# Kernel tuning notes

Measured on AMD Instinct MI355X. Metric: run time of the kernel, lower is better.

The kernel has to match this reference:

```python
import jax, jax.numpy as jnp
import numpy as np

N, T, D_KQ, E_KQ, D_V, E_V, H = 2, 2048, 1024, 1024, 1024, 1024, 16


def setup_inputs() -> dict:
    key = jax.random.key(0)
    ks = jax.random.split(key, 12)
    def lin(k, fan_in, fan_out):
        return jax.random.normal(k, (fan_in, fan_out), jnp.float32) * (1.0 / np.sqrt(fan_in))
    return {
        "kq": jax.random.normal(ks[0], (N, T, D_KQ), jnp.float32),
        "v": jax.random.normal(ks[1], (N, T, D_V), jnp.float32),
        "Wk": lin(ks[2], D_KQ, E_KQ), "bk": jnp.zeros((E_KQ,), jnp.float32),
        "Wq": lin(ks[3], D_KQ, E_KQ), "bq": jnp.zeros((E_KQ,), jnp.float32),
        "Wv": lin(ks[4], D_V, E_V),   "bv": jnp.zeros((E_V,), jnp.float32),
        "W1": lin(ks[5], E_V, 4 * E_V), "b1": jnp.zeros((4 * E_V,), jnp.float32),
        "W2": lin(ks[6], 4 * E_V, E_V), "b2": jnp.zeros((E_V,), jnp.float32),
    }


def _shifted_causal_mask(T):
    # triu(-inf, diagonal=0): block j >= i (strictly-past attention), except [0,0] unmasked
    row = jnp.arange(T)[:, None]
    col = jnp.arange(T)[None, :]
    mask = jnp.where(col < row, 0.0, -jnp.inf).astype(jnp.float32)
    return mask.at[0, 0].set(0.0)


def reference(kq, v, Wk, bk, Wq, bq, Wv, bv, W1, b1, W2, b2):
    n, T, _ = kq.shape
    hd_kq = E_KQ // H
    hd_v = E_V // H
    # projections -> [n, H, T, hd]
    k = (kq @ Wk + bk).reshape(n, T, H, hd_kq).transpose(0, 2, 1, 3)
    q = (kq @ Wq + bq).reshape(n, T, H, hd_kq).transpose(0, 2, 1, 3)
    vv = (v @ Wv + bv).reshape(n, T, H, hd_v).transpose(0, 2, 1, 3)
    # NOTE: no 1/sqrt(d) scaling, faithful to source
    scores = jnp.einsum("bhqd,bhkd->bhqk", q, k) + _shifted_causal_mask(T)
    attn = jax.nn.softmax(scores, axis=-1)
    out = jnp.einsum("bhqk,bhkd->bhqd", attn, vv)
    out = out.transpose(0, 2, 1, 3).reshape(n, T, E_V)
    # GELU FFN (torch nn.GELU default = exact erf form)
    h = jax.nn.gelu(out @ W1 + b1, approximate=False)
    return h @ W2 + b2
```

## Files before the change

kernel.cpp:

```cpp
#include <hip/hip_runtime.h>

typedef short bf16x8 __attribute__((ext_vector_type(8)));
typedef unsigned short u16x8 __attribute__((ext_vector_type(8)));
typedef float f32x4 __attribute__((ext_vector_type(4)));
typedef unsigned short u16;

#define MFMA16(a, b, c) __builtin_amdgcn_mfma_f32_16x16x32_bf16((a), (b), (c), 0, 0, 0)
#define VMCNT0() asm volatile("s_waitcnt vmcnt(0)" ::: "memory")

__device__ __forceinline__ u16 bf16_rtn(float f) {
  unsigned u = __float_as_uint(f);
  u += 0x7fffu + ((u >> 16) & 1u);
  return (u16)(u >> 16);
}
__device__ __forceinline__ float bf16_to_f(u16 h) {
  return __uint_as_float(((unsigned)h) << 16);
}
__device__ __forceinline__ void splitf(float f, u16& hi, u16& lo) {
  hi = bf16_rtn(f);
  lo = bf16_rtn(f - bf16_to_f(hi));
}
__device__ __forceinline__ void gload16(const void* g, void* l) {
  __builtin_amdgcn_global_load_lds(
      (const __attribute__((address_space(1))) unsigned int*)g,
      (__attribute__((address_space(3))) unsigned int*)l, 16, 0, 0);
}
__device__ __forceinline__ float exp2_hw(float x) {
  float r;
  asm("v_exp_f32 %0, %1" : "=v"(r) : "v"(x));
  return r;
}
__device__ __forceinline__ void swz_bid(int& bx, int& by) {
  int gx = gridDim.x;
  int lin = (int)blockIdx.y * gx + (int)blockIdx.x;
  int cpx = (gx * (int)gridDim.y) >> 3;
  int nl = (lin & 7) * cpx + (lin >> 3);
  bx = nl % gx;
  by = nl / gx;
}

__global__ void k_cvt(const float* __restrict__ a, const float* __restrict__ b,
                      u16* __restrict__ hi, u16* __restrict__ lo,
                      u16* __restrict__ vb) {
  int i = blockIdx.x * blockDim.x + threadIdx.x;
  const int N4 = 1 << 20;
  if (i < N4) {
    float4 v4 = ((const float4*)a)[i];
    ushort4 h, l;
    splitf(v4.x, h.x, l.x);
    splitf(v4.y, h.y, l.y);
    splitf(v4.z, h.z, l.z);
    splitf(v4.w, h.w, l.w);
    ((ushort4*)hi)[i] = h;
    ((ushort4*)lo)[i] = l;
  } else {
    int j = i - N4;
    float4 v4 = ((const float4*)b)[j];
    ushort4 h;
    h.x = bf16_rtn(v4.x);
    h.y = bf16_rtn(v4.y);
    h.z = bf16_rtn(v4.z);
    h.w = bf16_rtn(v4.w);
    ((ushort4*)vb)[j] = h;
  }
}

template <int SPLIT>
__global__ void k_tconv(const float* __restrict__ in, u16* __restrict__ hi,
                        u16* __restrict__ lo, int R, int C) {
  __shared__ float tile[32][33];
  int c0 = blockIdx.x * 32, r0 = blockIdx.y * 32;
  int tx = threadIdx.x & 31, ty = threadIdx.x >> 5;
#pragma unroll
  for (int i = 0; i < 4; ++i)
    tile[ty + i * 8][tx] = in[(size_t)(r0 + ty + i * 8) * C + c0 + tx];
  __syncthreads();
#pragma unroll
  for (int i = 0; i < 4; ++i) {
    float v = tile[tx][ty + i * 8];
    size_t o = (size_t)(c0 + ty + i * 8) * R + r0 + tx;
    if (SPLIT) {
      u16 h, l;
      splitf(v, h, l);
      hi[o] = h;
      lo[o] = l;
    } else {
      hi[o] = bf16_rtn(v);
    }
  }
}

template <int GELU, int OUT, int BN>
__global__ __launch_bounds__(256) void k_gemm(
    const u16* __restrict__ A, const u16* __restrict__ B,
    const float* __restrict__ bias, void* __restrict__ C0,
    int M, int Nc, int K) {
  extern __shared__ u16 sm[];
  const int NB = BN / 32;
  const int BUFE = 8192 + BN * 64;

  int bx, by;
  swz_bid(bx, by);
  int m0 = by * 128, n0 = bx * BN;
  int t = threadIdx.x, lane = t & 63, w = t >> 6;
  int wr = (w >> 1) * 64, wc = (w & 1) * (BN / 2);
  int li = lane & 15, g = lane >> 4;
  int lrow = lane >> 3, lcg = lane & 7;

  f32x4 acc[4][4] = {};
  const int nk = K >> 6;

  auto stage = [&](int kb, int buf) {
    int k0 = kb * 64;
    u16* base = sm + buf * BUFE;
#pragma unroll
    for (int j = 0; j < 4; ++j) {
      int jj = w * 4 + j;
      int row = jj * 8 + lrow;
      int cg = lcg ^ (row & 7);
      gload16(A + (size_t)(m0 + row) * K + k0 + cg * 8, base + jj * 512);
    }
#pragma unroll
    for (int j = 0; j < NB; ++j) {
      int jj = w * NB + j;
      int row = jj * 8 + lrow;
      int cg = lcg ^ (row & 7);
      gload16(B + (size_t)(n0 + row) * K + k0 + cg * 8, base + 8192 + jj * 512);
    }
  };

  stage(0, 0);
  VMCNT0();
  __syncthreads();

  int cur = 0;
  for (int kb = 0; kb < nk; ++kb) {
    if (kb + 1 < nk) stage(kb + 1, cur ^ 1);
    const u16* bs = sm + cur * BUFE;
#pragma unroll
    for (int kk = 0; kk < 2; ++kk) {
      bf16x8 af[4], bf[4];
#pragma unroll
      for (int i = 0; i < 4; ++i) {
        int row = wr + i * 16 + li;
        af[i] = *(const bf16x8*)&bs[row * 64 + (((kk * 4 + g) ^ (li & 7)) << 3)];
      }
#pragma unroll
      for (int b = 0; b < NB; ++b) {
        int row = wc + b * 16 + li;
        bf[b] = *(const bf16x8*)&bs[8192 + row * 64 + (((kk * 4 + g) ^ (li & 7)) << 3)];
      }
#pragma unroll
      for (int a = 0; a < 4; ++a)
#pragma unroll
        for (int b = 0; b < NB; ++b) acc[a][b] = MFMA16(af[a], bf[b], acc[a][b]);
    }
    VMCNT0();
    __syncthreads();
    cur ^= 1;
  }

#pragma unroll
  for (int a = 0; a < 4; ++a)
#pragma unroll
    for (int b = 0; b < NB; ++b)
#pragma unroll
      for (int r = 0; r < 4; ++r) {
        int row = m0 + wr + a * 16 + g * 4 + r;
        int col = n0 + wc + b * 16 + li;
        float v = acc[a][b][r] + bias[col];
        if (GELU) v = 0.5f * v * (1.0f + erff(v * 0.70710678118654752f));
        if (OUT == 0) {
          ((float*)C0)[(size_t)row * Nc + col] = v;
        } else if (OUT == 1) {
          ((u16*)C0)[(size_t)row * Nc + col] = bf16_rtn(v);
        } else if (OUT == 5) {
          int nn = row >> 11, tt = row & 2047, kbb = tt >> 6, tr = tt & 63;
          int hq = col >> 6, d = col & 63;
          size_t base = (((size_t)nn * 16 + hq) * 32 + kbb) * 8192 + 4096;
          size_t ov = base + d * 64 + (tr & 7) + (((tr >> 3) ^ (d & 7)) << 3);
          ((u16*)C0)[ov] = bf16_rtn(v);
        }
      }
}

__global__ __launch_bounds__(256) void k_gemm_s(
    const u16* __restrict__ Ahi, const u16* __restrict__ Alo,
    const u16* __restrict__ Bhi, const u16* __restrict__ Blo,
    const float* __restrict__ bias, const float* __restrict__ bias2,
    void* __restrict__ C0, void* __restrict__ C1, void* __restrict__ C2,
    int M, int Nc, int K) {
  extern __shared__ u16 sm[];
  const int BUFE = 16384;

  int bx, by;
  swz_bid(bx, by);
  int m0 = by * 128, n0 = bx * 128;
  int t = threadIdx.x, lane = t & 63, w = t >> 6;
  int wr = (w >> 1) * 64, wc = (w & 1) * 64;
  int li = lane & 15, g = lane >> 4;
  int srow = lane >> 2, scol = (lane & 3) * 8;

  f32x4 acc[4][4] = {};
  const int nk = K >> 5;

  auto stage = [&](int kb, int buf) {
    int k0 = kb * 32;
    int bo = buf * BUFE;
#pragma unroll
    for (int c = 0; c < 2; ++c) {
      int row = w * 32 + c * 16 + srow;
      int ldso = bo + w * 1024 + c * 512;
      gload16(Ahi + (size_t)(m0 + row) * K + k0 + scol, sm + ldso);
      gload16(Bhi + (size_t)(n0 + row) * K + k0 + scol, sm + 4096 + ldso);
      gload16(Alo + (size_t)(m0 + row) * K + k0 + scol, sm + 8192 + ldso);
      gload16(Blo + (size_t)(n0 + row) * K + k0 + scol, sm + 12288 + ldso);
    }
  };

  stage(0, 0);
  VMCNT0();
  __syncthreads();

  int cur = 0;
  for (int kb = 0; kb < nk; ++kb) {
    if (kb + 1 < nk) stage(kb + 1, cur ^ 1);
    const u16* lA = sm + cur * BUFE;
    bf16x8 af[4], bfr[4], afl[4], bfl[4];
#pragma unroll
    for (int i = 0; i < 4; ++i) {
      af[i] = *(const bf16x8*)&lA[(wr + i * 16 + li) * 32 + g * 8];
      bfr[i] = *(const bf16x8*)&lA[4096 + (wc + i * 16 + li) * 32 + g * 8];
      afl[i] = *(const bf16x8*)&lA[8192 + (wr + i * 16 + li) * 32 + g * 8];
      bfl[i] = *(const bf16x8*)&lA[12288 + (wc + i * 16 + li) * 32 + g * 8];
    }
#pragma unroll
    for (int a = 0; a < 4; ++a)
#pragma unroll
      for (int b = 0; b < 4; ++b) {
        acc[a][b] = MFMA16(af[a], bfr[b], acc[a][b]);
        acc[a][b] = MFMA16(af[a], bfl[b], acc[a][b]);
        acc[a][b] = MFMA16(afl[a], bfr[b], acc[a][b]);
      }
    VMCNT0();
    __syncthreads();
    cur ^= 1;
  }

#pragma unroll
  for (int a = 0; a < 4; ++a)
#pragma unroll
    for (int b = 0; b < 4; ++b)
#pragma unroll
      for (int r = 0; r < 4; ++r) {
        int row = m0 + wr + a * 16 + g * 4 + r;
        int col = n0 + wc + b * 16 + li;
        float bb = col < 1024 ? bias[col] : bias2[col - 1024];
        float v = acc[a][b][r] + bb;
        if (col < 1024) {
          int nn = row >> 11, tt = row & 2047, kbb = tt >> 6, tr = tt & 63;
          int hq = col >> 6, d = col & 63, ks = d >> 5, dc = d & 31;
          size_t base = (((size_t)nn * 16 + hq) * 32 + kbb) * 8192;
          size_t oh = base + ks * 2048 + tr * 32 + (dc & 7) +
                      (((dc >> 3) ^ ((tr >> 1) & 3)) << 3);
          ((u16*)C0)[oh] = bf16_rtn(v);
        } else {
          int cq = col - 1024;
          float vq = v * 1.4426950408889634f;
          u16 hh, ll;
          splitf(vq, hh, ll);
          size_t off = (((size_t)(row >> 11) * 16 + (cq >> 6)) * 2048 + (row & 2047)) * 64 + (cq & 63);
          ((u16*)C1)[off] = hh;
          ((u16*)C2)[off] = ll;
        }
      }
}

__global__ __launch_bounds__(512) void k_attn(
    const u16* __restrict__ Qh, const u16* __restrict__ Ql,
    const u16* __restrict__ KV, u16* __restrict__ out) {
  const int T = 2048, HD = 64, H = 16, E = 1024;
  int hc = blockIdx.x;
  int h = hc & 15, n = hc >> 4;
  int qq = 15 - (int)blockIdx.y;
  __shared__ u16 KB[2][8192];
  __shared__ u16 P[2][128][36];
  int t = threadIdx.x, lane = t & 63, w = t >> 6;
  int li = lane & 15, g = lane >> 4;

  const size_t nh = (size_t)n * H + h;
  const u16* qhb = Qh + (nh * 2048 + (size_t)qq * 128) * 64;
  const u16* qlb = Ql + (nh * 2048 + (size_t)qq * 128) * 64;
  const u16* kvb = KV + nh * 32 * 8192;

  bf16x8 qh[2], ql[2];
#pragma unroll
  for (int ks = 0; ks < 2; ++ks) {
    qh[ks] = *(const bf16x8*)&qhb[(w * 16 + li) * 64 + ks * 32 + g * 8];
    ql[ks] = *(const bf16x8*)&qlb[(w * 16 + li) * 64 + ks * 32 + g * 8];
  }

#pragma unroll
  for (int j = 0; j < 2; ++j)
    gload16(kvb + (w * 2 + j) * 512 + lane * 8, &KB[0][(w * 2 + j) * 512]);
  VMCNT0();
  __syncthreads();

  float lr[4] = {0.f, 0.f, 0.f, 0.f};
  f32x4 O[4] = {};
  int cur = 0;
  const int nkb = 2 * qq + 2;

  for (int kb = 0; kb < nkb; ++kb) {
    if (kb + 1 < nkb) {
      const u16* src = kvb + (size_t)(kb + 1) * 8192 + (w * 2) * 512 + lane * 8;
#pragma unroll
      for (int j = 0; j < 2; ++j)
        gload16(src + j * 512, &KB[cur ^ 1][(w * 2 + j) * 512]);
    }

    f32x4 s[4] = {};
#pragma unroll
    for (int ks = 0; ks < 2; ++ks)
#pragma unroll
      for (int c = 0; c < 4; ++c) {
        int jr = c * 16 + li;
        int sw = (jr >> 1) & 3;
        bf16x8 kh = *(const bf16x8*)&KB[cur][ks * 2048 + jr * 32 + ((g ^ sw) << 3)];
        s[c] = MFMA16(qh[ks], kh, s[c]);
        s[c] = MFMA16(ql[ks], kh, s[c]);
      }

    if (kb >= 2 * qq) {
#pragma unroll
      for (int c = 0; c < 4; ++c)
#pragma unroll
        for (int r = 0; r < 4; ++r) {
          int i = qq * 128 + w * 16 + g * 4 + r;
          int j = kb * 64 + c * 16 + li;
          if (!(j < i || (i == 0 && j == 0))) s[c][r] = -INFINITY;
        }
    }

#pragma unroll
    for (int c = 0; c < 4; ++c)
#pragma unroll
      for (int r = 0; r < 4; ++r) {
        float p = exp2_hw(s[c][r]);
        s[c][r] = p;
        lr[r] += p;
      }

#pragma unroll
    for (int c = 0; c < 4; ++c)
#pragma unroll
      for (int r = 0; r < 4; ++r)
        P[c >> 1][w * 16 + g * 4 + r][(c & 1) * 16 + li] = bf16_rtn(s[c][r]);

#pragma unroll
    for (int ks = 0; ks < 2; ++ks) {
      bf16x8 pa = *(const bf16x8*)&P[ks][w * 16 + li][g * 8];
#pragma unroll
      for (int c = 0; c < 4; ++c) {
        int d = c * 16 + li;
        int tc = ks * 4 + g;
        bf16x8 vb = *(const bf16x8*)&KB[cur][4096 + d * 64 + ((tc ^ (d & 7)) << 3)];
        O[c] = MFMA16(pa, vb, O[c]);
      }
    }
    VMCNT0();
    __syncthreads();
    cur ^= 1;
  }

#pragma unroll
  for (int off = 1; off < 16; off <<= 1)
#pragma unroll
    for (int r = 0; r < 4; ++r) lr[r] += __shfl_xor(lr[r], off, 16);

#pragma unroll
  for (int c = 0; c < 4; ++c)
#pragma unroll
    for (int r = 0; r < 4; ++r) {
      float v = O[c][r] / lr[r];
      size_t row = (size_t)n * T + qq * 128 + w * 16 + g * 4 + r;
      out[row * E + h * HD + c * 16 + li] = bf16_rtn(v);
    }
}

extern "C" void kernel_launch(void* const* d_in, const int* in_sizes, int n_in,
                              void* d_out, int out_size, void* d_ws, size_t ws_size,
                              hipStream_t stream) {
  const float* kq = (const float*)d_in[0];
  const float* v = (const float*)d_in[1];
  const float* Wk = (const float*)d_in[2];
  const float* bk = (const float*)d_in[3];
  const float* Wq = (const float*)d_in[4];
  const float* bq = (const float*)d_in[5];
  const float* Wv = (const float*)d_in[6];
  const float* bv = (const float*)d_in[7];
  const float* W1 = (const float*)d_in[8];
  const float* b1 = (const float*)d_in[9];
  const float* W2 = (const float*)d_in[10];
  const float* b2 = (const float*)d_in[11];
  float* outp = (float*)d_out;

  char* ws = (char*)d_ws;
  u16* kq_hi = (u16*)(ws + 0);
  u16* kq_lo = (u16*)(ws + 8388608);
  u16* v_bf = (u16*)(ws + 16777216);
  u16* hbuf = (u16*)(ws + 0);
  u16* WkqT_hi = (u16*)(ws + 33554432);
  u16* WkqT_lo = (u16*)(ws + 37748736);
  u16* WvT = (u16*)(ws + 41943040);
  u16* W1T = (u16*)(ws + 44040192);
  u16* W2T = (u16*)(ws + 52428800);
  u16* Qh = (u16*)(ws + 60817408);
  u16* Ql = (u16*)(ws + 69206016);
  u16* KV = (u16*)(ws + 77594624);
  u16* attn_o = (u16*)(ws + 102760448);

  k_cvt<<<8192, 256, 0, stream>>>(kq, v, kq_hi, kq_lo, v_bf);
  k_tconv<1><<<dim3(32, 32), 256, 0, stream>>>(Wk, WkqT_hi, WkqT_lo, 1024, 1024);
  k_tconv<1><<<dim3(32, 32), 256, 0, stream>>>(Wq, WkqT_hi + (1 << 20), WkqT_lo + (1 << 20), 1024, 1024);
  k_tconv<0><<<dim3(32, 32), 256, 0, stream>>>(Wv, WvT, nullptr, 1024, 1024);
  k_tconv<0><<<dim3(128, 32), 256, 0, stream>>>(W1, W1T, nullptr, 1024, 4096);
  k_tconv<0><<<dim3(32, 128), 256, 0, stream>>>(W2, W2T, nullptr, 4096, 1024);

  k_gemm_s<<<dim3(16, 32), 256, 65536, stream>>>(
      kq_hi, kq_lo, WkqT_hi, WkqT_lo, bk, bq, KV, Qh, Ql, 4096, 2048, 1024);
  k_gemm<0, 5, 64><<<dim3(16, 32), 256, 49152, stream>>>(
      v_bf, WvT, bv, KV, 4096, 1024, 1024);

  k_attn<<<dim3(32, 16), 512, 0, stream>>>(Qh, Ql, KV, attn_o);

  k_gemm<1, 1, 128><<<dim3(32, 32), 256, 65536, stream>>>(
      attn_o, W1T, b1, hbuf, 4096, 4096, 1024);
  k_gemm<0, 0, 64><<<dim3(16, 32), 256, 49152, stream>>>(
      hbuf, W2T, b2, outp, 4096, 1024, 4096);
}
```

Measured before the change: 250.5 us.

## Triple-buffer GEMM and attention loads, drop activation lo-split, fuse weight transposes

Moves the GEMMs and the attention kernel from double to triple buffering in LDS, with a partial vmcnt wait so two stages are in flight at once. The K/Q projection no longer splits the kq activation into hi/lo, which removes one MFMA per tile and a quarter of the staged loads but lowers input precision. The Wk/Wq/Wv transposes merge into one launch, the k_gemm_s LDS layout gains an XOR swizzle, and the FFN1 GEMM tile width drops from 128 to 64. Static shared arrays replace dynamic LDS, and the larger footprint may reduce occupancy.

```diff
diff --git a/kernel.cpp b/kernel.cpp
--- a/kernel.cpp
+++ b/kernel.cpp
@@ -7,6 +7,7 @@
 
 #define MFMA16(a, b, c) __builtin_amdgcn_mfma_f32_16x16x32_bf16((a), (b), (c), 0, 0, 0)
 #define VMCNT0() asm volatile("s_waitcnt vmcnt(0)" ::: "memory")
+#define VMCNTN(n) asm volatile("s_waitcnt vmcnt(" #n ")" ::: "memory")
 
 __device__ __forceinline__ u16 bf16_rtn(float f) {
   unsigned u = __float_as_uint(f);
@@ -40,54 +41,60 @@
 }
 
 __global__ void k_cvt(const float* __restrict__ a, const float* __restrict__ b,
-                      u16* __restrict__ hi, u16* __restrict__ lo,
-                      u16* __restrict__ vb) {
+                      u16* __restrict__ ah, u16* __restrict__ vb) {
   int i = blockIdx.x * blockDim.x + threadIdx.x;
   const int N4 = 1 << 20;
-  if (i < N4) {
-    float4 v4 = ((const float4*)a)[i];
-    ushort4 h, l;
-    splitf(v4.x, h.x, l.x);
-    splitf(v4.y, h.y, l.y);
-    splitf(v4.z, h.z, l.z);
-    splitf(v4.w, h.w, l.w);
-    ((ushort4*)hi)[i] = h;
-    ((ushort4*)lo)[i] = l;
-  } else {
-    int j = i - N4;
-    float4 v4 = ((const float4*)b)[j];
-    ushort4 h;
-    h.x = bf16_rtn(v4.x);
-    h.y = bf16_rtn(v4.y);
-    h.z = bf16_rtn(v4.z);
-    h.w = bf16_rtn(v4.w);
-    ((ushort4*)vb)[j] = h;
-  }
-}
-
-template <int SPLIT>
-__global__ void k_tconv(const float* __restrict__ in, u16* __restrict__ hi,
-                        u16* __restrict__ lo, int R, int C) {
+  const float4 v4 = (i < N4) ? ((const float4*)a)[i] : ((const float4*)b)[i - N4];
+  ushort4 h;
+  h.x = bf16_rtn(v4.x);
+  h.y = bf16_rtn(v4.y);
+  h.z = bf16_rtn(v4.z);
+  h.w = bf16_rtn(v4.w);
+  if (i < N4)
+    ((ushort4*)ah)[i] = h;
+  else
+    ((ushort4*)vb)[i - N4] = h;
+}
+
+__global__ void k_tconvW(const float* __restrict__ Wk, const float* __restrict__ Wq,
+                         const float* __restrict__ Wv, u16* __restrict__ hi,
+                         u16* __restrict__ lo, u16* __restrict__ wvt) {
+  int z = blockIdx.z;
+  const float* in = (z == 0) ? Wk : (z == 1) ? Wq : Wv;
   __shared__ float tile[32][33];
   int c0 = blockIdx.x * 32, r0 = blockIdx.y * 32;
   int tx = threadIdx.x & 31, ty = threadIdx.x >> 5;
 #pragma unroll
   for (int i = 0; i < 4; ++i)
+    tile[ty + i * 8][tx] = in[(size_t)(r0 + ty + i * 8) * 1024 + c0 + tx];
+  __syncthreads();
+#pragma unroll
+  for (int i = 0; i < 4; ++i) {
+    float v = tile[tx][ty + i * 8];
+    size_t o = (size_t)(c0 + ty + i * 8) * 1024 + r0 + tx;
+    if (z < 2) {
+      u16 h, l;
+      splitf(v, h, l);
+      hi[(size_t)z * 1048576 + o] = h;
+      lo[(size_t)z * 1048576 + o] = l;
+    } else {
+      wvt[o] = bf16_rtn(v);
+    }
+  }
+}
+
+__global__ void k_tconv(const float* __restrict__ in, u16* __restrict__ hi,
+                        int R, int C) {
+  __shared__ float tile[32][33];
+  int c0 = blockIdx.x * 32, r0 = blockIdx.y * 32;
+  int tx = threadIdx.x & 31, ty = threadIdx.x >> 5;
+#pragma unroll
+  for (int i = 0; i < 4; ++i)
     tile[ty + i * 8][tx] = in[(size_t)(r0 + ty + i * 8) * C + c0 + tx];
   __syncthreads();
 #pragma unroll
-  for (int i = 0; i < 4; ++i) {
-    float v = tile[tx][ty + i * 8];
-    size_t o = (size_t)(c0 + ty + i * 8) * R + r0 + tx;
-    if (SPLIT) {
-      u16 h, l;
-      splitf(v, h, l);
-      hi[o] = h;
-      lo[o] = l;
-    } else {
-      hi[o] = bf16_rtn(v);
-    }
-  }
+  for (int i = 0; i < 4; ++i)
+    hi[(size_t)(c0 + ty + i * 8) * R + r0 + tx] = bf16_rtn(tile[tx][ty + i * 8]);
 }
 
 template <int GELU, int OUT, int BN>
@@ -95,9 +102,9 @@
     const u16* __restrict__ A, const u16* __restrict__ B,
     const float* __restrict__ bias, void* __restrict__ C0,
     int M, int Nc, int K) {
-  extern __shared__ u16 sm[];
   const int NB = BN / 32;
   const int BUFE = 8192 + BN * 64;
+  __shared__ u16 sm[3 * BUFE];
 
   int bx, by;
   swz_bid(bx, by);
@@ -107,7 +114,7 @@
   int li = lane & 15, g = lane >> 4;
   int lrow = lane >> 3, lcg = lane & 7;
 
-  f32x4 acc[4][4] = {};
+  f32x4 acc[4][NB] = {};
   const int nk = K >> 6;
 
   auto stage = [&](int kb, int buf) {
@@ -130,16 +137,20 @@
   };
 
   stage(0, 0);
-  VMCNT0();
+  stage(1, 1);
+  VMCNTN(6);
   __syncthreads();
 
   int cur = 0;
   for (int kb = 0; kb < nk; ++kb) {
-    if (kb + 1 < nk) stage(kb + 1, cur ^ 1);
+    int stb = cur + 2;
+    if (stb >= 3) stb -= 3;
+    if (kb + 2 < nk) stage(kb + 2, stb);
+
     const u16* bs = sm + cur * BUFE;
 #pragma unroll
     for (int kk = 0; kk < 2; ++kk) {
-      bf16x8 af[4], bf[4];
+      bf16x8 af[4], bf[NB];
 #pragma unroll
       for (int i = 0; i < 4; ++i) {
         int row = wr + i * 16 + li;
@@ -155,9 +166,13 @@
 #pragma unroll
         for (int b = 0; b < NB; ++b) acc[a][b] = MFMA16(af[a], bf[b], acc[a][b]);
     }
-    VMCNT0();
+    if (kb + 2 < nk) {
+      VMCNTN(6);
+    } else {
+      VMCNT0();
+    }
     __syncthreads();
-    cur ^= 1;
+    cur = (cur == 2) ? 0 : cur + 1;
   }
 
 #pragma unroll
@@ -185,13 +200,12 @@
 }
 
 __global__ __launch_bounds__(256) void k_gemm_s(
-    const u16* __restrict__ Ahi, const u16* __restrict__ Alo,
-    const u16* __restrict__ Bhi, const u16* __restrict__ Blo,
-    const float* __restrict__ bias, const float* __restrict__ bias2,
-    void* __restrict__ C0, void* __restrict__ C1, void* __restrict__ C2,
-    int M, int Nc, int K) {
-  extern __shared__ u16 sm[];
-  const int BUFE = 16384;
+    const u16* __restrict__ Ahi, const u16* __restrict__ Bhi,
+    const u16* __restrict__ Blo, const float* __restrict__ bias,
+    const float* __restrict__ bias2, void* __restrict__ C0,
+    void* __restrict__ C1, void* __restrict__ C2, int M, int Nc, int K) {
+  const int BUFE = 12288;
+  __shared__ u16 sm[3 * BUFE];
 
   int bx, by;
   swz_bid(bx, by);
@@ -199,40 +213,44 @@
   int t = threadIdx.x, lane = t & 63, w = t >> 6;
   int wr = (w >> 1) * 64, wc = (w & 1) * 64;
   int li = lane & 15, g = lane >> 4;
-  int srow = lane >> 2, scol = (lane & 3) * 8;
+  int srow = lane >> 2;
+  int sc = ((lane & 3) ^ ((srow >> 1) & 3)) * 8;
 
   f32x4 acc[4][4] = {};
   const int nk = K >> 5;
 
   auto stage = [&](int kb, int buf) {
     int k0 = kb * 32;
-    int bo = buf * BUFE;
+    u16* base = sm + buf * BUFE;
 #pragma unroll
     for (int c = 0; c < 2; ++c) {
       int row = w * 32 + c * 16 + srow;
-      int ldso = bo + w * 1024 + c * 512;
-      gload16(Ahi + (size_t)(m0 + row) * K + k0 + scol, sm + ldso);
-      gload16(Bhi + (size_t)(n0 + row) * K + k0 + scol, sm + 4096 + ldso);
-      gload16(Alo + (size_t)(m0 + row) * K + k0 + scol, sm + 8192 + ldso);
-      gload16(Blo + (size_t)(n0 + row) * K + k0 + scol, sm + 12288 + ldso);
+      int ldso = w * 1024 + c * 512;
+      gload16(Ahi + (size_t)(m0 + row) * K + k0 + sc, base + ldso);
+      gload16(Bhi + (size_t)(n0 + row) * K + k0 + sc, base + 4096 + ldso);
+      gload16(Blo + (size_t)(n0 + row) * K + k0 + sc, base + 8192 + ldso);
     }
   };
 
   stage(0, 0);
-  VMCNT0();
+  stage(1, 1);
+  VMCNTN(6);
   __syncthreads();
 
   int cur = 0;
   for (int kb = 0; kb < nk; ++kb) {
-    if (kb + 1 < nk) stage(kb + 1, cur ^ 1);
-    const u16* lA = sm + cur * BUFE;
-    bf16x8 af[4], bfr[4], afl[4], bfl[4];
+    int stb = cur + 2;
+    if (stb >= 3) stb -= 3;
+    if (kb + 2 < nk) stage(kb + 2, stb);
+
+    const u16* bs = sm + cur * BUFE;
+    bf16x8 af[4], bfr[4], bfl[4];
 #pragma unroll
     for (int i = 0; i < 4; ++i) {
-      af[i] = *(const bf16x8*)&lA[(wr + i * 16 + li) * 32 + g * 8];
-      bfr[i] = *(const bf16x8*)&lA[4096 + (wc + i * 16 + li) * 32 + g * 8];
-      afl[i] = *(const bf16x8*)&lA[8192 + (wr + i * 16 + li) * 32 + g * 8];
-      bfl[i] = *(const bf16x8*)&lA[12288 + (wc + i * 16 + li) * 32 + g * 8];
+      int swz = (g ^ ((li >> 1) & 3)) << 3;
+      af[i] = *(const bf16x8*)&bs[(wr + i * 16 + li) * 32 + swz];
+      bfr[i] = *(const bf16x8*)&bs[4096 + (wc + i * 16 + li) * 32 + swz];
+      bfl[i] = *(const bf16x8*)&bs[8192 + (wc + i * 16 + li) * 32 + swz];
     }
 #pragma unroll
     for (int a = 0; a < 4; ++a)
@@ -240,11 +258,14 @@
       for (int b = 0; b < 4; ++b) {
         acc[a][b] = MFMA16(af[a], bfr[b], acc[a][b]);
         acc[a][b] = MFMA16(af[a], bfl[b], acc[a][b]);
-        acc[a][b] = MFMA16(afl[a], bfr[b], acc[a][b]);
-      }
-    VMCNT0();
+      }
+    if (kb + 2 < nk) {
+      VMCNTN(6);
+    } else {
+      VMCNT0();
+    }
     __syncthreads();
-    cur ^= 1;
+    cur = (cur == 2) ? 0 : cur + 1;
   }
 
 #pragma unroll
@@ -283,7 +304,7 @@
   int hc = blockIdx.x;
   int h = hc & 15, n = hc >> 4;
   int qq = 15 - (int)blockIdx.y;
-  __shared__ u16 KB[2][8192];
+  __shared__ u16 KB[3][8192];
   __shared__ u16 P[2][128][36];
   int t = threadIdx.x, lane = t & 63, w = t >> 6;
   int li = lane & 15, g = lane >> 4;
@@ -303,7 +324,10 @@
 #pragma unroll
   for (int j = 0; j < 2; ++j)
     gload16(kvb + (w * 2 + j) * 512 + lane * 8, &KB[0][(w * 2 + j) * 512]);
-  VMCNT0();
+#pragma unroll
+  for (int j = 0; j < 2; ++j)
+    gload16(kvb + 8192 + (w * 2 + j) * 512 + lane * 8, &KB[1][(w * 2 + j) * 512]);
+  VMCNTN(2);
   __syncthreads();
 
   float lr[4] = {0.f, 0.f, 0.f, 0.f};
@@ -312,11 +336,13 @@
   const int nkb = 2 * qq + 2;
 
   for (int kb = 0; kb < nkb; ++kb) {
-    if (kb + 1 < nkb) {
-      const u16* src = kvb + (size_t)(kb + 1) * 8192 + (w * 2) * 512 + lane * 8;
+    int stb = cur + 2;
+    if (stb >= 3) stb -= 3;
+    if (kb + 2 < nkb) {
+      const u16* src = kvb + (size_t)(kb + 2) * 8192 + (w * 2) * 512 + lane * 8;
 #pragma unroll
       for (int j = 0; j < 2; ++j)
-        gload16(src + j * 512, &KB[cur ^ 1][(w * 2 + j) * 512]);
+        gload16(src + j * 512, &KB[stb][(w * 2 + j) * 512]);
     }
 
     f32x4 s[4] = {};
@@ -368,9 +394,13 @@
         O[c] = MFMA16(pa, vb, O[c]);
       }
     }
-    VMCNT0();
+    if (kb + 2 < nkb) {
+      VMCNTN(2);
+    } else {
+      VMCNT0();
+    }
     __syncthreads();
-    cur ^= 1;
+    cur = (cur == 2) ? 0 : cur + 1;
   }
 
 #pragma unroll
@@ -407,8 +437,7 @@
 
   char* ws = (char*)d_ws;
   u16* kq_hi = (u16*)(ws + 0);
-  u16* kq_lo = (u16*)(ws + 8388608);
-  u16* v_bf = (u16*)(ws + 16777216);
+  u16* v_bf = (u16*)(ws + 8388608);
   u16* hbuf = (u16*)(ws + 0);
   u16* WkqT_hi = (u16*)(ws + 33554432);
   u16* WkqT_lo = (u16*)(ws + 37748736);
@@ -420,22 +449,20 @@
   u16* KV = (u16*)(ws + 77594624);
   u16* attn_o = (u16*)(ws + 102760448);
 
-  k_cvt<<<8192, 256, 0, stream>>>(kq, v, kq_hi, kq_lo, v_bf);
-  k_tconv<1><<<dim3(32, 32), 256, 0, stream>>>(Wk, WkqT_hi, WkqT_lo, 1024, 1024);
-  k_tconv<1><<<dim3(32, 32), 256, 0, stream>>>(Wq, WkqT_hi + (1 << 20), WkqT_lo + (1 << 20), 1024, 1024);
-  k_tconv<0><<<dim3(32, 32), 256, 0, stream>>>(Wv, WvT, nullptr, 1024, 1024);
-  k_tconv<0><<<dim3(128, 32), 256, 0, stream>>>(W1, W1T, nullptr, 1024, 4096);
-  k_tconv<0><<<dim3(32, 128), 256, 0, stream>>>(W2, W2T, nullptr, 4096, 1024);
-
-  k_gemm_s<<<dim3(16, 32), 256, 65536, stream>>>(
-      kq_hi, kq_lo, WkqT_hi, WkqT_lo, bk, bq, KV, Qh, Ql, 4096, 2048, 1024);
-  k_gemm<0, 5, 64><<<dim3(16, 32), 256, 49152, stream>>>(
+  k_cvt<<<8192, 256, 0, stream>>>(kq, v, kq_hi, v_bf);
+  k_tconvW<<<dim3(32, 32, 3), 256, 0, stream>>>(Wk, Wq, Wv, WkqT_hi, WkqT_lo, WvT);
+  k_tconv<<<dim3(128, 32), 256, 0, stream>>>(W1, W1T, 1024, 4096);
+  k_tconv<<<dim3(32, 128), 256, 0, stream>>>(W2, W2T, 4096, 1024);
+
+  k_gemm_s<<<dim3(16, 32), 256, 0, stream>>>(
+      kq_hi, WkqT_hi, WkqT_lo, bk, bq, KV, Qh, Ql, 4096, 2048, 1024);
+  k_gemm<0, 5, 64><<<dim3(16, 32), 256, 0, stream>>>(
       v_bf, WvT, bv, KV, 4096, 1024, 1024);
 
   k_attn<<<dim3(32, 16), 512, 0, stream>>>(Qh, Ql, KV, attn_o);
 
-  k_gemm<1, 1, 128><<<dim3(32, 32), 256, 65536, stream>>>(
+  k_gemm<1, 1, 64><<<dim3(64, 32), 256, 0, stream>>>(
       attn_o, W1T, b1, hbuf, 4096, 4096, 1024);
-  k_gemm<0, 0, 64><<<dim3(16, 32), 256, 49152, stream>>>(
+  k_gemm<0, 0, 64><<<dim3(16, 32), 256, 0, stream>>>(
       hbuf, W2T, b2, outp, 4096, 1024, 4096);
 }
```

Measured after the change: 239.9 us. -4.2%, faster.
